# Kernel optimization log

Measured on AMD Instinct MI355X. Metric: run time of the kernel, lower is better.

## Reference

```python
import jax, jax.numpy as jnp
import numpy as np

B, T, H, W = 64, 128, 64, 64
K = 3          # conv kernel size
NH = 64        # hidden_dim == n_qubits (required for the gating math to broadcast)
IN = 1         # input_dim (scalar conv feature per frame)
NC = 10        # num_classes


def setup_inputs() -> dict:
    key = jax.random.key(0)
    ks = jax.random.split(key, 32)
    i = iter(range(32))

    def lin(kw, kb, fan_in, fan_out):
        s = 1.0 / np.sqrt(fan_in)
        w = jax.random.uniform(kw, (fan_out, fan_in), jnp.float32, -s, s)
        b = jax.random.uniform(kb, (fan_out,), jnp.float32, -s, s)
        return w, b

    inp = {"images": jax.random.normal(ks[next(i)], (B, T, 1, H, W), jnp.float32)}
    inp["threshold"] = jnp.float32(0.5)
    s = 1.0 / np.sqrt(K * K)
    inp["conv_w"] = jax.random.uniform(ks[next(i)], (1, 1, K, K), jnp.float32, -s, s)
    inp["conv_b"] = jax.random.uniform(ks[next(i)], (1,), jnp.float32, -s, s)
    for g in ("f", "i", "u", "o"):
        w, b = lin(ks[next(i)], ks[next(i)], IN + NH, NH)
        inp[f"fc_{g}_w"], inp[f"fc_{g}_b"] = w, b
        lw, lb = lin(ks[next(i)], ks[next(i)], NH, NH)
        ew, eb = lin(ks[next(i)], ks[next(i)], NH, NH)
        inp[f"q_{g}_lw"], inp[f"q_{g}_lb"] = lw, lb
        inp[f"q_{g}_ew"], inp[f"q_{g}_eb"] = ew, eb
    inp["cls_w"], inp["cls_b"] = lin(ks[next(i)], ks[next(i)], NH, NC)
    return inp


def _qlayer(x, lw, lb, ew, eb):
    out = jnp.tanh(x @ lw.T + lb)
    return out * jax.nn.sigmoid(out @ ew.T + eb)


def reference(images, threshold, conv_w, conv_b,
              fc_f_w, fc_f_b, fc_i_w, fc_i_b, fc_u_w, fc_u_b, fc_o_w, fc_o_b,
              q_f_lw, q_f_lb, q_f_ew, q_f_eb,
              q_i_lw, q_i_lb, q_i_ew, q_i_eb,
              q_u_lw, q_u_lb, q_u_ew, q_u_eb,
              q_o_lw, q_o_lb, q_o_ew, q_o_eb,
              cls_w, cls_b):
    b, t, c, h, w = images.shape
    nh = q_f_lw.shape[0]
    # ConvFilter over all frames at once (vectorized across batch*time)
    x = images.reshape(b * t, c, h, w)
    logits = jax.lax.conv_general_dilated(
        x, conv_w, (1, 1), "VALID",
        dimension_numbers=("NCHW", "OIHW", "NCHW")) + conv_b[None, :, None, None]
    feat = jax.nn.sigmoid(logits - threshold).mean(axis=(2, 3))  # [B*T, 1]
    seq = feat.reshape(b, t, 1).transpose(1, 0, 2)               # [T, B, 1]

    def step(carry, xt):
        hx, cx = carry
        comb = jnp.concatenate([xt, hx], axis=1)                 # [B, 1+NH]
        f = jax.nn.sigmoid(_qlayer(comb @ fc_f_w.T + fc_f_b, q_f_lw, q_f_lb, q_f_ew, q_f_eb))
        i = jax.nn.sigmoid(_qlayer(comb @ fc_i_w.T + fc_i_b, q_i_lw, q_i_lb, q_i_ew, q_i_eb))
        g = jnp.tanh(_qlayer(comb @ fc_u_w.T + fc_u_b, q_u_lw, q_u_lb, q_u_ew, q_u_eb))
        o = jax.nn.sigmoid(_qlayer(comb @ fc_o_w.T + fc_o_b, q_o_lw, q_o_lb, q_o_ew, q_o_eb))
        cx = f * cx + i * g
        hx = o * jnp.tanh(cx)
        return (hx, cx), hx

    h0 = jnp.zeros((b, nh), images.dtype)
    c0 = jnp.zeros((b, nh), images.dtype)
    _, outs = jax.lax.scan(step, (h0, c0), seq)                  # [T, B, NH]
    return outs @ cls_w.T + cls_b                                # [T, B, NC]
```

## Files before the change

### kernel.cpp

```cpp
#include <hip/hip_runtime.h>

#define T_ 128
#define B_ 64
#define NH_ 64
#define NC_ 10

__device__ __forceinline__ float sigmoid_f(float x) {
    return 1.0f / (1.0f + __expf(-x));
}
__device__ __forceinline__ float tanh_f(float x) {
    return 1.0f - 2.0f / (1.0f + __expf(2.0f * x));
}

__global__ __launch_bounds__(256) void conv_feat(const float* __restrict__ img,
                                                 const float* __restrict__ cw,
                                                 const float* __restrict__ cb,
                                                 const float* __restrict__ thr,
                                                 float* __restrict__ feat) {
    __shared__ __align__(16) float im[64 * 64];
    const int f = blockIdx.x;
    const int tid = threadIdx.x;
    const float* src = img + (size_t)f * 4096;
#pragma unroll
    for (int i = 0; i < 4; i++) {
        *(float4*)&im[(i * 256 + tid) * 4] = *(const float4*)&src[(i * 256 + tid) * 4];
    }
    const float w0 = cw[0], w1 = cw[1], w2 = cw[2], w3 = cw[3], w4 = cw[4],
                w5 = cw[5], w6 = cw[6], w7 = cw[7], w8 = cw[8];
    const float bias = cb[0] - thr[0];
    __syncthreads();

    float sum = 0.0f;
#pragma unroll
    for (int i = 0; i < 16; i++) {
        int idx = i * 256 + tid;
        if (idx < 62 * 62) {
            int oy = idx / 62;
            int ox = idx - oy * 62;
            const float* p = &im[oy * 64 + ox];
            float acc = bias;
            acc = fmaf(p[0],   w0, acc);
            acc = fmaf(p[1],   w1, acc);
            acc = fmaf(p[2],   w2, acc);
            acc = fmaf(p[64],  w3, acc);
            acc = fmaf(p[65],  w4, acc);
            acc = fmaf(p[66],  w5, acc);
            acc = fmaf(p[128], w6, acc);
            acc = fmaf(p[129], w7, acc);
            acc = fmaf(p[130], w8, acc);
            sum += sigmoid_f(acc);
        }
    }
#pragma unroll
    for (int off = 32; off >= 1; off >>= 1) sum += __shfl_down(sum, off, 64);
    __shared__ float wsum[4];
    const int wv = tid >> 6, ln = tid & 63;
    if (ln == 0) wsum[wv] = sum;
    __syncthreads();
    if (tid == 0) feat[f] = (wsum[0] + wsum[1] + wsum[2] + wsum[3]) * (1.0f / 3844.0f);
}

struct FuseArgs {
    const float* fcw[4];
    const float* fcb[4];
    const float* lw[4];
    const float* lb[4];
};

__global__ __launch_bounds__(256) void fuse_kernel(FuseArgs a, float* __restrict__ Aall,
                                                   float* __restrict__ Vall,
                                                   float* __restrict__ Call) {
    const int g = blockIdx.x;
    const float* fcw = a.fcw[g];
    const float* fcb = a.fcb[g];
    const float* lw  = a.lw[g];
    const float* lb  = a.lb[g];
    __shared__ float fcs[64 * 65];
    __shared__ float fbs[64];
    for (int i = threadIdx.x; i < 64 * 65; i += 256) fcs[i] = fcw[i];
    if (threadIdx.x < 64) fbs[threadIdx.x] = fcb[threadIdx.x];
    __syncthreads();

    const int n = threadIdx.x >> 2;
    const int j0 = (threadIdx.x & 3) * 16;
    float lrow[64];
#pragma unroll
    for (int k = 0; k < 64; k++) lrow[k] = lw[n * 64 + k];

    for (int j = j0; j < j0 + 16; j++) {
        float s = 0.0f;
#pragma unroll
        for (int k = 0; k < 64; k++) s = fmaf(lrow[k], fcs[k * 65 + j + 1], s);
        Aall[(g * 64 + n) * 64 + j] = s;
    }
    if ((threadIdx.x & 3) == 0) {
        float sv = 0.0f, sc = 0.0f;
#pragma unroll
        for (int k = 0; k < 64; k++) {
            sv = fmaf(lrow[k], fcs[k * 65], sv);
            sc = fmaf(lrow[k], fbs[k], sc);
        }
        Vall[g * 64 + n] = sv;
        Call[g * 64 + n] = sc + lb[n];
    }
}

__global__ __launch_bounds__(256, 1) void recur(
    const float* __restrict__ feat, const float* __restrict__ Aall,
    const float* __restrict__ Vall, const float* __restrict__ Call,
    const float* __restrict__ ew_f, const float* __restrict__ eb_f,
    const float* __restrict__ ew_i, const float* __restrict__ eb_i,
    const float* __restrict__ ew_u, const float* __restrict__ eb_u,
    const float* __restrict__ ew_o, const float* __restrict__ eb_o,
    float* __restrict__ outs) {
    const int b = blockIdx.x;
    const int tid = threadIdx.x;
    const int g = tid >> 6, n = tid & 63;
    const float* ew  = (g == 0) ? ew_f : (g == 1) ? ew_i : (g == 2) ? ew_u : ew_o;
    const float* ebp = (g == 0) ? eb_f : (g == 1) ? eb_i : (g == 2) ? eb_u : eb_o;

    float W1[64], W2[64];
#pragma unroll
    for (int k4 = 0; k4 < 16; k4++) {
        float4 av = *(const float4*)&Aall[tid * 64 + k4 * 4];
        W1[k4 * 4 + 0] = av.x; W1[k4 * 4 + 1] = av.y;
        W1[k4 * 4 + 2] = av.z; W1[k4 * 4 + 3] = av.w;
        float4 ev = *(const float4*)&ew[n * 64 + k4 * 4];
        W2[k4 * 4 + 0] = ev.x; W2[k4 * 4 + 1] = ev.y;
        W2[k4 * 4 + 2] = ev.z; W2[k4 * 4 + 3] = ev.w;
    }
    const float vj = Vall[tid], cj = Call[tid], ebj = ebp[n];

    __shared__ __align__(16) float hxs[64];
    __shared__ __align__(16) float qs[256];
    __shared__ __align__(16) float acts[256];
    __shared__ float xts[T_];
    for (int i = tid; i < T_; i += 256) xts[i] = feat[b * T_ + i];
    if (tid < 64) hxs[tid] = 0.0f;
    float cx = 0.0f;
    __syncthreads();

    for (int t = 0; t < T_; t++) {
        float a0 = 0, a1 = 0, a2 = 0, a3 = 0;
#pragma unroll
        for (int k4 = 0; k4 < 16; k4++) {
            float4 h = *(const float4*)&hxs[k4 * 4];
            a0 = fmaf(W1[k4 * 4 + 0], h.x, a0);
            a1 = fmaf(W1[k4 * 4 + 1], h.y, a1);
            a2 = fmaf(W1[k4 * 4 + 2], h.z, a2);
            a3 = fmaf(W1[k4 * 4 + 3], h.w, a3);
        }
        const float q = tanh_f(fmaf(xts[t], vj, cj) + ((a0 + a1) + (a2 + a3)));
        qs[tid] = q;
        __syncthreads();

        float s0 = 0, s1 = 0, s2 = 0, s3 = 0;
#pragma unroll
        for (int k4 = 0; k4 < 16; k4++) {
            float4 qv = *(const float4*)&qs[(g << 6) + k4 * 4];
            s0 = fmaf(W2[k4 * 4 + 0], qv.x, s0);
            s1 = fmaf(W2[k4 * 4 + 1], qv.y, s1);
            s2 = fmaf(W2[k4 * 4 + 2], qv.z, s2);
            s3 = fmaf(W2[k4 * 4 + 3], qv.w, s3);
        }
        const float z = q * sigmoid_f(((s0 + s1) + (s2 + s3)) + ebj);
        const float act = (g == 2) ? tanh_f(z) : sigmoid_f(z);
        acts[tid] = act;
        __syncthreads();

        if (tid < 64) {
            const float ff = acts[tid], ii = acts[64 + tid],
                        uu = acts[128 + tid], oo = acts[192 + tid];
            cx = fmaf(ff, cx, ii * uu);
            const float h = oo * tanh_f(cx);
            hxs[tid] = h;
            outs[((size_t)t * B_ + b) * NH_ + tid] = h;
        }
        __syncthreads();
    }
}

__global__ __launch_bounds__(256) void classify(const float* __restrict__ outs,
                                                const float* __restrict__ cw,
                                                const float* __restrict__ cbias,
                                                float* __restrict__ out) {
    const int tid = threadIdx.x;
    const int r = tid >> 6, ln = tid & 63;
    const int row = blockIdx.x * 4 + r;
    const float h = outs[(size_t)row * 64 + ln];
    float p[10];
#pragma unroll
    for (int c = 0; c < 10; c++) p[c] = h * cw[c * 64 + ln];
#pragma unroll
    for (int off = 32; off >= 1; off >>= 1) {
#pragma unroll
        for (int c = 0; c < 10; c++) p[c] += __shfl_xor(p[c], off, 64);
    }
    if (ln < 10) out[(size_t)row * 10 + ln] = p[ln] + cbias[ln];
}

extern "C" void kernel_launch(void* const* d_in, const int* in_sizes, int n_in,
                              void* d_out, int out_size, void* d_ws, size_t ws_size,
                              hipStream_t stream) {
    const float* images = (const float*)d_in[0];
    const float* thr    = (const float*)d_in[1];
    const float* convw  = (const float*)d_in[2];
    const float* convb  = (const float*)d_in[3];
    const float* fcw[4]; const float* fcb[4]; const float* lw[4]; const float* lb[4];
    const float* ew[4];  const float* eb[4];
    for (int g = 0; g < 4; g++) {
        int base = 4 + g * 6;
        fcw[g] = (const float*)d_in[base + 0];
        fcb[g] = (const float*)d_in[base + 1];
        lw[g]  = (const float*)d_in[base + 2];
        lb[g]  = (const float*)d_in[base + 3];
        ew[g]  = (const float*)d_in[base + 4];
        eb[g]  = (const float*)d_in[base + 5];
    }
    const float* clsw = (const float*)d_in[28];
    const float* clsb = (const float*)d_in[29];

    float* ws   = (float*)d_ws;
    float* feat = ws;
    float* Aall = ws + 8192;
    float* Vall = ws + 24576;
    float* Call = ws + 24832;
    float* outs = ws + 25088;

    conv_feat<<<8192, 256, 0, stream>>>(images, convw, convb, thr, feat);

    FuseArgs fa;
    for (int g = 0; g < 4; g++) {
        fa.fcw[g] = fcw[g]; fa.fcb[g] = fcb[g];
        fa.lw[g] = lw[g];   fa.lb[g] = lb[g];
    }
    fuse_kernel<<<4, 256, 0, stream>>>(fa, Aall, Vall, Call);

    recur<<<B_, 256, 0, stream>>>(feat, Aall, Vall, Call,
                                  ew[0], eb[0], ew[1], eb[1],
                                  ew[2], eb[2], ew[3], eb[3], outs);

    classify<<<2048, 256, 0, stream>>>(outs, clsw, clsb, (float*)d_out);
}
```

Baseline: 181.0 us.

## Register-tile conv, readlane matvecs in recurrence, fuse classifier into recurrent kernel

The conv kernel now has each thread compute 16 adjacent outputs of one row from register-cached row segments in a padded shared buffer, replacing per-output division and nine scattered LDS loads. The recurrent kernel broadcasts h and q through readlane instead of shared memory, cutting two barriers per timestep down to one by double-buffering the activations and having every wave redundantly update the cell state. The classifier is fused into the recurrent kernel using a shared-memory history of h, which removes one launch and the global round trip of the hidden outputs. The cost is more redundant work across the four waves and extra shared memory per block.

New measurement: 211.0 us. 16.5% more time.

```diff
diff --git a/kernel.cpp b/kernel.cpp
--- a/kernel.cpp
+++ b/kernel.cpp
@@ -11,53 +11,69 @@
 __device__ __forceinline__ float tanh_f(float x) {
     return 1.0f - 2.0f / (1.0f + __expf(2.0f * x));
 }
-
+__device__ __forceinline__ float readlane_f(float v, int lane) {
+    return __int_as_float(__builtin_amdgcn_readlane(__float_as_int(v), lane));
+}
+
+#define IMP 68
 __global__ __launch_bounds__(256) void conv_feat(const float* __restrict__ img,
                                                  const float* __restrict__ cw,
                                                  const float* __restrict__ cb,
                                                  const float* __restrict__ thr,
                                                  float* __restrict__ feat) {
-    __shared__ __align__(16) float im[64 * 64];
-    const int f = blockIdx.x;
+    __shared__ __align__(16) float im[64 * IMP];
+    __shared__ float wsum[4];
     const int tid = threadIdx.x;
-    const float* src = img + (size_t)f * 4096;
+    const float* src = img + (size_t)blockIdx.x * 4096;
 #pragma unroll
     for (int i = 0; i < 4; i++) {
-        *(float4*)&im[(i * 256 + tid) * 4] = *(const float4*)&src[(i * 256 + tid) * 4];
+        const int idx = i * 256 + tid;
+        const int row = idx >> 4, c4 = idx & 15;
+        *(float4*)&im[row * IMP + c4 * 4] = *(const float4*)&src[idx * 4];
     }
     const float w0 = cw[0], w1 = cw[1], w2 = cw[2], w3 = cw[3], w4 = cw[4],
                 w5 = cw[5], w6 = cw[6], w7 = cw[7], w8 = cw[8];
     const float bias = cb[0] - thr[0];
     __syncthreads();
 
+    const int r  = tid >> 2;
+    const int c0 = (tid & 3) * 16;
     float sum = 0.0f;
-#pragma unroll
-    for (int i = 0; i < 16; i++) {
-        int idx = i * 256 + tid;
-        if (idx < 62 * 62) {
-            int oy = idx / 62;
-            int ox = idx - oy * 62;
-            const float* p = &im[oy * 64 + ox];
-            float acc = bias;
-            acc = fmaf(p[0],   w0, acc);
-            acc = fmaf(p[1],   w1, acc);
-            acc = fmaf(p[2],   w2, acc);
-            acc = fmaf(p[64],  w3, acc);
-            acc = fmaf(p[65],  w4, acc);
-            acc = fmaf(p[66],  w5, acc);
-            acc = fmaf(p[128], w6, acc);
-            acc = fmaf(p[129], w7, acc);
-            acc = fmaf(p[130], w8, acc);
-            sum += sigmoid_f(acc);
-        }
+    if (r < 62) {
+        const int ncols = (c0 == 48) ? 14 : 16;
+        float acc[16];
+#pragma unroll
+        for (int x = 0; x < 16; x++) acc[x] = bias;
+#pragma unroll
+        for (int dr = 0; dr < 3; dr++) {
+            float rb[20];
+#pragma unroll
+            for (int j = 0; j < 5; j++) {
+                float4 v = *(const float4*)&im[(r + dr) * IMP + c0 + j * 4];
+                rb[j * 4 + 0] = v.x; rb[j * 4 + 1] = v.y;
+                rb[j * 4 + 2] = v.z; rb[j * 4 + 3] = v.w;
+            }
+            const float k0 = (dr == 0) ? w0 : (dr == 1) ? w3 : w6;
+            const float k1 = (dr == 0) ? w1 : (dr == 1) ? w4 : w7;
+            const float k2 = (dr == 0) ? w2 : (dr == 1) ? w5 : w8;
+#pragma unroll
+            for (int x = 0; x < 16; x++) {
+                acc[x] = fmaf(rb[x], k0, acc[x]);
+                acc[x] = fmaf(rb[x + 1], k1, acc[x]);
+                acc[x] = fmaf(rb[x + 2], k2, acc[x]);
+            }
+        }
+#pragma unroll
+        for (int x = 0; x < 16; x++)
+            if (x < ncols) sum += sigmoid_f(acc[x]);
     }
 #pragma unroll
     for (int off = 32; off >= 1; off >>= 1) sum += __shfl_down(sum, off, 64);
-    __shared__ float wsum[4];
     const int wv = tid >> 6, ln = tid & 63;
     if (ln == 0) wsum[wv] = sum;
     __syncthreads();
-    if (tid == 0) feat[f] = (wsum[0] + wsum[1] + wsum[2] + wsum[3]) * (1.0f / 3844.0f);
+    if (tid == 0)
+        feat[blockIdx.x] = (wsum[0] + wsum[1] + wsum[2] + wsum[3]) * (1.0f / 3844.0f);
 }
 
 struct FuseArgs {
@@ -112,7 +128,8 @@
     const float* __restrict__ ew_i, const float* __restrict__ eb_i,
     const float* __restrict__ ew_u, const float* __restrict__ eb_u,
     const float* __restrict__ ew_o, const float* __restrict__ eb_o,
-    float* __restrict__ outs) {
+    const float* __restrict__ cls_w, const float* __restrict__ cls_b,
+    float* __restrict__ out) {
     const int b = blockIdx.x;
     const int tid = threadIdx.x;
     const int g = tid >> 6, n = tid & 63;
@@ -131,72 +148,69 @@
     }
     const float vj = Vall[tid], cj = Call[tid], ebj = ebp[n];
 
-    __shared__ __align__(16) float hxs[64];
-    __shared__ __align__(16) float qs[256];
-    __shared__ __align__(16) float acts[256];
+    __shared__ __align__(16) float acts[2][4][64];
     __shared__ float xts[T_];
+    __shared__ float hist[T_ * 65];
+    __shared__ float cwts[NC_ * 65 + NC_];
+
     for (int i = tid; i < T_; i += 256) xts[i] = feat[b * T_ + i];
-    if (tid < 64) hxs[tid] = 0.0f;
-    float cx = 0.0f;
+    for (int i = tid; i < NC_ * 64; i += 256) {
+        int c = i >> 6, k = i & 63;
+        cwts[c * 65 + k] = cls_w[i];
+    }
+    if (tid < NC_) cwts[NC_ * 65 + tid] = cls_b[tid];
+    float h_reg = 0.0f, cx = 0.0f;
     __syncthreads();
 
     for (int t = 0; t < T_; t++) {
+        const float xt = xts[t];
+
         float a0 = 0, a1 = 0, a2 = 0, a3 = 0;
 #pragma unroll
         for (int k4 = 0; k4 < 16; k4++) {
-            float4 h = *(const float4*)&hxs[k4 * 4];
-            a0 = fmaf(W1[k4 * 4 + 0], h.x, a0);
-            a1 = fmaf(W1[k4 * 4 + 1], h.y, a1);
-            a2 = fmaf(W1[k4 * 4 + 2], h.z, a2);
-            a3 = fmaf(W1[k4 * 4 + 3], h.w, a3);
-        }
-        const float q = tanh_f(fmaf(xts[t], vj, cj) + ((a0 + a1) + (a2 + a3)));
-        qs[tid] = q;
-        __syncthreads();
+            const int k = k4 * 4;
+            a0 = fmaf(W1[k + 0], readlane_f(h_reg, k + 0), a0);
+            a1 = fmaf(W1[k + 1], readlane_f(h_reg, k + 1), a1);
+            a2 = fmaf(W1[k + 2], readlane_f(h_reg, k + 2), a2);
+            a3 = fmaf(W1[k + 3], readlane_f(h_reg, k + 3), a3);
+        }
+        const float q = tanh_f(fmaf(xt, vj, cj) + ((a0 + a1) + (a2 + a3)));
 
         float s0 = 0, s1 = 0, s2 = 0, s3 = 0;
 #pragma unroll
         for (int k4 = 0; k4 < 16; k4++) {
-            float4 qv = *(const float4*)&qs[(g << 6) + k4 * 4];
-            s0 = fmaf(W2[k4 * 4 + 0], qv.x, s0);
-            s1 = fmaf(W2[k4 * 4 + 1], qv.y, s1);
-            s2 = fmaf(W2[k4 * 4 + 2], qv.z, s2);
-            s3 = fmaf(W2[k4 * 4 + 3], qv.w, s3);
+            const int k = k4 * 4;
+            s0 = fmaf(W2[k + 0], readlane_f(q, k + 0), s0);
+            s1 = fmaf(W2[k + 1], readlane_f(q, k + 1), s1);
+            s2 = fmaf(W2[k + 2], readlane_f(q, k + 2), s2);
+            s3 = fmaf(W2[k + 3], readlane_f(q, k + 3), s3);
         }
         const float z = q * sigmoid_f(((s0 + s1) + (s2 + s3)) + ebj);
         const float act = (g == 2) ? tanh_f(z) : sigmoid_f(z);
-        acts[tid] = act;
+
+        acts[t & 1][g][n] = act;
         __syncthreads();
-
-        if (tid < 64) {
-            const float ff = acts[tid], ii = acts[64 + tid],
-                        uu = acts[128 + tid], oo = acts[192 + tid];
-            cx = fmaf(ff, cx, ii * uu);
-            const float h = oo * tanh_f(cx);
-            hxs[tid] = h;
-            outs[((size_t)t * B_ + b) * NH_ + tid] = h;
-        }
-        __syncthreads();
-    }
-}
-
-__global__ __launch_bounds__(256) void classify(const float* __restrict__ outs,
-                                                const float* __restrict__ cw,
-                                                const float* __restrict__ cbias,
-                                                float* __restrict__ out) {
-    const int tid = threadIdx.x;
-    const int r = tid >> 6, ln = tid & 63;
-    const int row = blockIdx.x * 4 + r;
-    const float h = outs[(size_t)row * 64 + ln];
-    float p[10];
-#pragma unroll
-    for (int c = 0; c < 10; c++) p[c] = h * cw[c * 64 + ln];
-#pragma unroll
-    for (int off = 32; off >= 1; off >>= 1) {
-#pragma unroll
-        for (int c = 0; c < 10; c++) p[c] += __shfl_xor(p[c], off, 64);
-    }
-    if (ln < 10) out[(size_t)row * 10 + ln] = p[ln] + cbias[ln];
+        const float ff = acts[t & 1][0][n];
+        const float ii = acts[t & 1][1][n];
+        const float uu = acts[t & 1][2][n];
+        const float oo = acts[t & 1][3][n];
+
+        cx = fmaf(ff, cx, ii * uu);
+        h_reg = oo * tanh_f(cx);
+        if (g == 0) hist[t * 65 + n] = h_reg;
+    }
+    __syncthreads();
+
+#pragma unroll
+    for (int j = 0; j < 5; j++) {
+        const int o = j * 256 + tid;
+        const int r = o / 10;
+        const int c = o - r * 10;
+        float s = cwts[NC_ * 65 + c];
+#pragma unroll 16
+        for (int k = 0; k < 64; k++) s = fmaf(hist[r * 65 + k], cwts[c * 65 + k], s);
+        out[((size_t)r * B_ + b) * NC_ + c] = s;
+    }
 }
 
 extern "C" void kernel_launch(void* const* d_in, const int* in_sizes, int n_in,
@@ -225,7 +239,6 @@
     float* Aall = ws + 8192;
     float* Vall = ws + 24576;
     float* Call = ws + 24832;
-    float* outs = ws + 25088;
 
     conv_feat<<<8192, 256, 0, stream>>>(images, convw, convb, thr, feat);
 
@@ -238,7 +251,6 @@
 
     recur<<<B_, 256, 0, stream>>>(feat, Aall, Vall, Call,
                                   ew[0], eb[0], ew[1], eb[1],
-                                  ew[2], eb[2], ew[3], eb[3], outs);
-
-    classify<<<2048, 256, 0, stream>>>(outs, clsw, clsb, (float*)d_out);
-}
+                                  ew[2], eb[2], ew[3], eb[3],
+                                  clsw, clsb, (float*)d_out);
+}
```
